# Optimization experiments

Hardware: AMD Instinct MI355X
Metric: run time of the kernel (lower is better)

## Reference

```python
import jax, jax.numpy as jnp
import numpy as np

B, T, IN, H = 4096, 100, 140, 256


def setup_inputs() -> dict:
    key = jax.random.key(0)
    ks = jax.random.split(key, 13)
    s = 1.0 / np.sqrt(H)  # PyTorch LSTM/Linear default init scale
    u = lambda k, shape: jax.random.uniform(k, shape, jnp.float32, -s, s)
    return {
        "x": jax.random.normal(ks[0], (B, T, IN), jnp.float32),
        # LSTM layer 0 (input 140 -> hidden 256), PyTorch gate order i,f,g,o
        "W_ih0": u(ks[1], (4 * H, IN)),
        "W_hh0": u(ks[2], (4 * H, H)),
        "b_ih0": u(ks[3], (4 * H,)),
        "b_hh0": u(ks[4], (4 * H,)),
        # LSTM layer 1 (hidden 256 -> hidden 256)
        "W_ih1": u(ks[5], (4 * H, H)),
        "W_hh1": u(ks[6], (4 * H, H)),
        "b_ih1": u(ks[7], (4 * H,)),
        "b_hh1": u(ks[8], (4 * H,)),
        # advantage MLP: Linear(256,256) -> ReLU -> Linear(256,1)
        "W_a1": u(ks[9], (H, H)),
        "b_a1": u(ks[10], (H,)),
        "W_a2": u(ks[11], (1, H)),
        "b_a2": u(ks[12], (1,)),
    }


def _lstm_cell(xt, h, c, W_ih, W_hh, b):
    # xt: (B, in), h/c: (B, H). PyTorch gate order: i, f, g, o.
    g = xt @ W_ih.T + h @ W_hh.T + b
    i, f, gg, o = jnp.split(g, 4, axis=-1)
    c_new = jax.nn.sigmoid(f) * c + jax.nn.sigmoid(i) * jnp.tanh(gg)
    h_new = jax.nn.sigmoid(o) * jnp.tanh(c_new)
    return h_new, c_new


def reference(x, W_ih0, W_hh0, b_ih0, b_hh0, W_ih1, W_hh1, b_ih1, b_hh1,
              W_a1, b_a1, W_a2, b_a2):
    Bx = x.shape[0]
    b0 = b_ih0 + b_hh0
    b1 = b_ih1 + b_hh1

    def step(carry, xt):
        h0, c0, h1, c1 = carry
        h0, c0 = _lstm_cell(xt, h0, c0, W_ih0, W_hh0, b0)
        h1, c1 = _lstm_cell(h0, h1, c1, W_ih1, W_hh1, b1)
        a = jax.nn.relu(h1 @ W_a1.T + b_a1) @ W_a2.T + b_a2  # (B, 1)
        return (h0, c0, h1, c1), a[:, 0]

    init = tuple(jnp.zeros((Bx, H), x.dtype) for _ in range(4))
    _, outs = jax.lax.scan(step, init, jnp.swapaxes(x, 0, 1))  # (T, B)
    # Faithful to torch.cat(outputs).view(B, -1): flatten in t-major order,
    # then reshape to (B, T) (this scrambles batch/time exactly as the original).
    return outs.reshape(Bx, -1)
```

## Files before the change

kernel.cpp:

```cpp
#include <hip/hip_runtime.h>
#include <cstdint>
#include <cstddef>

#define T_STEPS 100
#define IN_DIM  140
#define HDIM    256
#define BTOT    4096
#define MROWS   16
#define NBLK    (BTOT/MROWS)
#define NTHR    512

typedef _Float16 f16;
typedef _Float16 f16x8 __attribute__((ext_vector_type(8)));
typedef float    f32x4 __attribute__((ext_vector_type(4)));

#define NS0 13
#define NS1 16
#define NSA 8
#define E0 (NS0*64*512)
#define E1 (NS1*64*512)
#define EA (NSA*16*512)
#define F16TOT (E0+E1+EA)
#define EB 2048
#define PREP_TOT (F16TOT+EB)

#define ACOLS 680
#define H0COL 160
#define H1COL 416

__device__ __forceinline__ float sigmoidf_(float x) {
    return 1.0f / (1.0f + __expf(-x));
}
__device__ __forceinline__ float tanhf_(float x) {
    return 1.0f - 2.0f / (__expf(2.0f * x) + 1.0f);
}

__global__ void prep(const float* __restrict__ Wih0, const float* __restrict__ Whh0,
                     const float* __restrict__ bih0, const float* __restrict__ bhh0,
                     const float* __restrict__ Wih1, const float* __restrict__ Whh1,
                     const float* __restrict__ bih1, const float* __restrict__ bhh1,
                     const float* __restrict__ Wa1,  f16* __restrict__ wsf,
                     float* __restrict__ wsb)
{
    int idx = blockIdx.x * 256 + threadIdx.x;
    if (idx < E0) {
        int e = idx & 7, l = (idx >> 3) & 63, fi = idx >> 9;
        int nt = fi & 63, ks = fi >> 6;
        int k = ks * 32 + ((l >> 4) << 3) + e;
        int n = nt * 16 + (l & 15);
        float v = (k < 160) ? (k < IN_DIM ? Wih0[n * IN_DIM + k] : 0.f)
                            : Whh0[n * HDIM + (k - 160)];
        wsf[idx] = (f16)v;
    } else if (idx < E0 + E1) {
        int i2 = idx - E0;
        int e = i2 & 7, l = (i2 >> 3) & 63, fi = i2 >> 9;
        int nt = fi & 63, ks = fi >> 6;
        int k = ks * 32 + ((l >> 4) << 3) + e;
        int n = nt * 16 + (l & 15);
        float v = (k < HDIM) ? Wih1[n * HDIM + k] : Whh1[n * HDIM + (k - HDIM)];
        wsf[idx] = (f16)v;
    } else if (idx < F16TOT) {
        int i3 = idx - (E0 + E1);
        int e = i3 & 7, l = (i3 >> 3) & 63, fi = i3 >> 9;
        int nt = fi & 15, ks = fi >> 4;
        int k = ks * 32 + ((l >> 4) << 3) + e;
        int j = nt * 16 + (l & 15);
        wsf[idx] = (f16)Wa1[j * HDIM + k];
    } else if (idx < PREP_TOT) {
        int i4 = idx - F16TOT;
        if (i4 < 1024) wsb[i4] = bih0[i4] + bhh0[i4];
        else           wsb[i4] = bih1[i4 - 1024] + bhh1[i4 - 1024];
    }
}

#define GLOAD_LDS(gsrc, ldst)                                              \
    __builtin_amdgcn_global_load_lds(                                      \
        (const __attribute__((address_space(1))) void*)(gsrc),             \
        (__attribute__((address_space(3))) void*)(ldst), 16, 0, 0)

#define BAR_LG do { asm volatile("s_waitcnt lgkmcnt(0)" ::: "memory");     \
                    __builtin_amdgcn_sched_barrier(0);                     \
                    __builtin_amdgcn_s_barrier();                          \
                    __builtin_amdgcn_sched_barrier(0); } while (0)

__device__ __forceinline__ f16x8 ldfrag(const f16* base, int f, int w, int l) {
    return *(const f16x8*)(base + ((size_t)(((f >> 1) << 4) + 2 * w + (f & 1)) << 9) + l * 8);
}

__global__ __launch_bounds__(NTHR) void lstm_mfma(
    const float* __restrict__ x, const f16* __restrict__ wsf,
    const float* __restrict__ wsb, const float* __restrict__ Wa2,
    const float* __restrict__ ba1, const float* __restrict__ ba2,
    float* __restrict__ out)
{
    __shared__ __align__(16) f16 A[MROWS][ACOLS];
    __shared__ __align__(16) f16 advL[8 * 16 * 512];
    __shared__ float red[8][MROWS];

    const int tid = threadIdx.x;
    const int l   = tid & 63;
    const int w   = tid >> 6;
    const int lm  = l & 15;
    const int lk  = (l >> 4) << 3;
    const int m0  = (l >> 4) << 2;
    const int row0 = blockIdx.x * MROWS;

    const f16* W0 = wsf;
    const f16* W1 = wsf + E0;
    const f16* WA = wsf + E0 + E1;

    for (int i = tid; i < MROWS * ACOLS; i += NTHR) ((f16*)A)[i] = (f16)0.f;

    const int u0 = (2 * w) * 16 + lm;
    const int u1 = (2 * w + 1) * 16 + lm;
    float b0v[2][4], b1v[2][4];
    #pragma unroll
    for (int g = 0; g < 4; g++) {
        b0v[0][g] = wsb[g * 256 + u0];          b0v[1][g] = wsb[g * 256 + u1];
        b1v[0][g] = wsb[1024 + g * 256 + u0];   b1v[1][g] = wsb[1024 + g * 256 + u1];
    }
    const float bAv[2]  = { ba1[u0], ba1[u1] };
    const float wa2v[2] = { Wa2[u0], Wa2[u1] };
    const float ba2v    = ba2[0];

    #pragma unroll
    for (int fi = 0; fi < 16; fi++) {
        const f16* src = WA + ((size_t)(((fi >> 1) << 4) + 2 * w + (fi & 1)) << 9) + l * 8;
        GLOAD_LDS(src, advL + (size_t)(w * 16 + fi) * 512);
    }

    float c0s[2][4], c1s[2][4];
    #pragma unroll
    for (int q = 0; q < 2; q++)
        #pragma unroll
        for (int r = 0; r < 4; r++) { c0s[q][r] = 0.f; c1s[q][r] = 0.f; }

    for (int i = tid; i < MROWS * IN_DIM; i += NTHR) {
        int b = i / IN_DIM, k = i - b * IN_DIM;
        A[b][k] = (f16)x[(size_t)(row0 + b) * (T_STEPS * IN_DIM) + k];
    }
    f16x8 cur[8];
    #pragma unroll
    for (int f = 0; f < 8; f++) cur[f] = ldfrag(W0, f, w, l);

    __syncthreads();

    #pragma unroll 1
    for (int t = 0; t < T_STEPS; t++) {
        f32x4 acc[2][4];
        #pragma unroll
        for (int q = 0; q < 2; q++)
            #pragma unroll
            for (int g = 0; g < 4; g++) {
                float b = b0v[q][g];
                acc[q][g] = (f32x4){b, b, b, b};
            }
        #pragma unroll 1
        for (int ks = 0; ks < NS0; ks++) {
            const f16* nb = (ks < NS0 - 1) ? (W0 + (size_t)(ks + 1) * (64 * 512)) : W1;
            f16x8 nxt[8];
            #pragma unroll
            for (int f = 0; f < 8; f++) nxt[f] = ldfrag(nb, f, w, l);
            f16x8 a0 = *(const f16x8*)&A[lm][ks * 32 + lk];
            #pragma unroll
            for (int g = 0; g < 4; g++)
                #pragma unroll
                for (int q = 0; q < 2; q++)
                    acc[q][g] = __builtin_amdgcn_mfma_f32_16x16x32_f16(a0, cur[g * 2 + q], acc[q][g], 0, 0, 0);
            #pragma unroll
            for (int f = 0; f < 8; f++) cur[f] = nxt[f];
        }

        f16 hnew[2][4];
        #pragma unroll
        for (int q = 0; q < 2; q++)
            #pragma unroll
            for (int r = 0; r < 4; r++) {
                float ig = sigmoidf_(acc[q][0][r]);
                float fg = sigmoidf_(acc[q][1][r]);
                float gv = tanhf_   (acc[q][2][r]);
                float og = sigmoidf_(acc[q][3][r]);
                float c  = fmaf(fg, c0s[q][r], ig * gv);
                c0s[q][r] = c;
                hnew[q][r] = (f16)(og * tanhf_(c));
            }
        BAR_LG;
        #pragma unroll
        for (int r = 0; r < 4; r++) {
            A[m0 + r][H0COL + u0] = hnew[0][r];
            A[m0 + r][H0COL + u1] = hnew[1][r];
        }
        BAR_LG;

        #pragma unroll
        for (int q = 0; q < 2; q++)
            #pragma unroll
            for (int g = 0; g < 4; g++) {
                float b = b1v[q][g];
                acc[q][g] = (f32x4){b, b, b, b};
            }
        #pragma unroll 1
        for (int ks = 0; ks < NS1; ks++) {
            const f16* nb = (ks < NS1 - 1) ? (W1 + (size_t)(ks + 1) * (64 * 512)) : W0;
            f16x8 nxt[8];
            #pragma unroll
            for (int f = 0; f < 8; f++) nxt[f] = ldfrag(nb, f, w, l);
            f16x8 a0 = *(const f16x8*)&A[lm][H0COL + ks * 32 + lk];
            #pragma unroll
            for (int g = 0; g < 4; g++)
                #pragma unroll
                for (int q = 0; q < 2; q++)
                    acc[q][g] = __builtin_amdgcn_mfma_f32_16x16x32_f16(a0, cur[g * 2 + q], acc[q][g], 0, 0, 0);
            #pragma unroll
            for (int f = 0; f < 8; f++) cur[f] = nxt[f];
        }

        #pragma unroll
        for (int q = 0; q < 2; q++)
            #pragma unroll
            for (int r = 0; r < 4; r++) {
                float ig = sigmoidf_(acc[q][0][r]);
                float fg = sigmoidf_(acc[q][1][r]);
                float gv = tanhf_   (acc[q][2][r]);
                float og = sigmoidf_(acc[q][3][r]);
                float c  = fmaf(fg, c1s[q][r], ig * gv);
                c1s[q][r] = c;
                hnew[q][r] = (f16)(og * tanhf_(c));
            }
        BAR_LG;
        #pragma unroll
        for (int r = 0; r < 4; r++) {
            A[m0 + r][H1COL + u0] = hnew[0][r];
            A[m0 + r][H1COL + u1] = hnew[1][r];
        }
        BAR_LG;

        f32x4 accA[2];
        #pragma unroll
        for (int q = 0; q < 2; q++) {
            float b = bAv[q];
            accA[q] = (f32x4){b, b, b, b};
        }
        #pragma unroll
        for (int ks = 0; ks < NSA; ks++) {
            f16x8 a0 = *(const f16x8*)&A[lm][H1COL + ks * 32 + lk];
            f16x8 bf0 = *(const f16x8*)(advL + (size_t)(w * 16 + 2 * ks + 0) * 512 + l * 8);
            f16x8 bf1 = *(const f16x8*)(advL + (size_t)(w * 16 + 2 * ks + 1) * 512 + l * 8);
            accA[0] = __builtin_amdgcn_mfma_f32_16x16x32_f16(a0, bf0, accA[0], 0, 0, 0);
            accA[1] = __builtin_amdgcn_mfma_f32_16x16x32_f16(a0, bf1, accA[1], 0, 0, 0);
        }

        {
            const int tn = (t + 1 < T_STEPS) ? (t + 1) : t;
            for (int i = tid; i < MROWS * IN_DIM; i += NTHR) {
                int b = i / IN_DIM, k = i - b * IN_DIM;
                A[b][k] = (f16)x[(size_t)(row0 + b) * (T_STEPS * IN_DIM) + (size_t)tn * IN_DIM + k];
            }
        }

        float s[4];
        #pragma unroll
        for (int r = 0; r < 4; r++)
            s[r] = fmaxf(accA[0][r], 0.f) * wa2v[0] + fmaxf(accA[1][r], 0.f) * wa2v[1];
        #pragma unroll
        for (int msk = 1; msk < 16; msk <<= 1)
            #pragma unroll
            for (int r = 0; r < 4; r++)
                s[r] += __shfl_xor(s[r], msk, 64);
        if (lm == 0) {
            #pragma unroll
            for (int r = 0; r < 4; r++) red[w][m0 + r] = s[r];
        }
        BAR_LG;
        if (tid < MROWS) {
            float o = ba2v;
            #pragma unroll
            for (int w2 = 0; w2 < 8; w2++) o += red[w2][tid];
            out[(size_t)t * BTOT + row0 + tid] = o;
        }
    }
}

extern "C" void kernel_launch(void* const* d_in, const int* in_sizes, int n_in,
                              void* d_out, int out_size, void* d_ws, size_t ws_size,
                              hipStream_t stream)
{
    const float* x    = (const float*)d_in[0];
    const float* Wih0 = (const float*)d_in[1];
    const float* Whh0 = (const float*)d_in[2];
    const float* bih0 = (const float*)d_in[3];
    const float* bhh0 = (const float*)d_in[4];
    const float* Wih1 = (const float*)d_in[5];
    const float* Whh1 = (const float*)d_in[6];
    const float* bih1 = (const float*)d_in[7];
    const float* bhh1 = (const float*)d_in[8];
    const float* Wa1  = (const float*)d_in[9];
    const float* ba1  = (const float*)d_in[10];
    const float* Wa2  = (const float*)d_in[11];
    const float* ba2  = (const float*)d_in[12];

    f16*   wsf = (f16*)d_ws;
    float* wsb = (float*)((char*)d_ws + (size_t)F16TOT * sizeof(f16));
    float* out = (float*)d_out;

    hipLaunchKernelGGL(prep, dim3(PREP_TOT / 256), dim3(256), 0, stream,
                       Wih0, Whh0, bih0, bhh0, Wih1, Whh1, bih1, bhh1, Wa1, wsf, wsb);
    hipLaunchKernelGGL(lstm_mfma, dim3(NBLK), dim3(NTHR), 0, stream,
                       x, wsf, wsb, Wa2, ba1, ba2, out);
}
```

Baseline: 1.998 ms.

## Double-buffer LSTM weight fragments two k-slices ahead and set waves_per_eu

Replaces the single-slice register prefetch (cur/nxt copy) with two alternating register buffers. Each global load now has a full k-slice of MFMA work to hide behind, and the register copy is gone. The k-loops are unrolled by two, and the boundary slices are hand-sequenced so the next layer's first two slices are prefetched. A waves_per_eu(2) attribute is added to steer register allocation. The extra fragment registers raise VGPR pressure, and any slip in the prefetch ordering at the layer boundaries would use the wrong weights.

```diff
diff --git a/kernel.cpp b/kernel.cpp
--- a/kernel.cpp
+++ b/kernel.cpp
@@ -23,6 +23,7 @@
 #define F16TOT (E0+E1+EA)
 #define EB 2048
 #define PREP_TOT (F16TOT+EB)
+#define SL (64*512)
 
 #define ACOLS 680
 #define H0COL 160
@@ -87,7 +88,9 @@
     return *(const f16x8*)(base + ((size_t)(((f >> 1) << 4) + 2 * w + (f & 1)) << 9) + l * 8);
 }
 
-__global__ __launch_bounds__(NTHR) void lstm_mfma(
+__global__ __launch_bounds__(NTHR)
+__attribute__((amdgpu_waves_per_eu(2)))
+void lstm_mfma(
     const float* __restrict__ x, const f16* __restrict__ wsf,
     const float* __restrict__ wsb, const float* __restrict__ Wa2,
     const float* __restrict__ ba1, const float* __restrict__ ba2,
@@ -139,9 +142,26 @@
         int b = i / IN_DIM, k = i - b * IN_DIM;
         A[b][k] = (f16)x[(size_t)(row0 + b) * (T_STEPS * IN_DIM) + k];
     }
-    f16x8 cur[8];
-    #pragma unroll
-    for (int f = 0; f < 8; f++) cur[f] = ldfrag(W0, f, w, l);
+
+    f16x8 bsE[8], bsO[8];
+
+#define LDSETX(ARR, BASE)                                                  \
+    do { _Pragma("unroll")                                                 \
+         for (int f = 0; f < 8; f++) ARR[f] = ldfrag((BASE), f, w, l);     \
+    } while (0)
+
+#define MFMA_SX(ARR, COL)                                                  \
+    do { f16x8 a0 = *(const f16x8*)&A[lm][(COL) + lk];                     \
+         _Pragma("unroll")                                                 \
+         for (int g = 0; g < 4; g++)                                       \
+             _Pragma("unroll")                                             \
+             for (int q = 0; q < 2; q++)                                   \
+                 acc[q][g] = __builtin_amdgcn_mfma_f32_16x16x32_f16(       \
+                     a0, ARR[g * 2 + q], acc[q][g], 0, 0, 0);              \
+    } while (0)
+
+    LDSETX(bsE, W0 + 0 * SL);
+    LDSETX(bsO, W0 + 1 * SL);
 
     __syncthreads();
 
@@ -156,20 +176,13 @@
                 acc[q][g] = (f32x4){b, b, b, b};
             }
         #pragma unroll 1
-        for (int ks = 0; ks < NS0; ks++) {
-            const f16* nb = (ks < NS0 - 1) ? (W0 + (size_t)(ks + 1) * (64 * 512)) : W1;
-            f16x8 nxt[8];
-            #pragma unroll
-            for (int f = 0; f < 8; f++) nxt[f] = ldfrag(nb, f, w, l);
-            f16x8 a0 = *(const f16x8*)&A[lm][ks * 32 + lk];
-            #pragma unroll
-            for (int g = 0; g < 4; g++)
-                #pragma unroll
-                for (int q = 0; q < 2; q++)
-                    acc[q][g] = __builtin_amdgcn_mfma_f32_16x16x32_f16(a0, cur[g * 2 + q], acc[q][g], 0, 0, 0);
-            #pragma unroll
-            for (int f = 0; f < 8; f++) cur[f] = nxt[f];
-        }
+        for (int j = 0; j < 5; j++) {
+            MFMA_SX(bsE, (2 * j) * 32);     LDSETX(bsE, W0 + (size_t)(2 * j + 2) * SL);
+            MFMA_SX(bsO, (2 * j + 1) * 32); LDSETX(bsO, W0 + (size_t)(2 * j + 3) * SL);
+        }
+        MFMA_SX(bsE, 10 * 32);  LDSETX(bsE, W0 + 12 * SL);
+        MFMA_SX(bsO, 11 * 32);  LDSETX(bsO, W1 + 1 * SL);
+        MFMA_SX(bsE, 12 * 32);  LDSETX(bsE, W1 + 0 * SL);
 
         f16 hnew[2][4];
         #pragma unroll
@@ -200,20 +213,12 @@
                 acc[q][g] = (f32x4){b, b, b, b};
             }
         #pragma unroll 1
-        for (int ks = 0; ks < NS1; ks++) {
-            const f16* nb = (ks < NS1 - 1) ? (W1 + (size_t)(ks + 1) * (64 * 512)) : W0;
-            f16x8 nxt[8];
-            #pragma unroll
-            for (int f = 0; f < 8; f++) nxt[f] = ldfrag(nb, f, w, l);
-            f16x8 a0 = *(const f16x8*)&A[lm][H0COL + ks * 32 + lk];
-            #pragma unroll
-            for (int g = 0; g < 4; g++)
-                #pragma unroll
-                for (int q = 0; q < 2; q++)
-                    acc[q][g] = __builtin_amdgcn_mfma_f32_16x16x32_f16(a0, cur[g * 2 + q], acc[q][g], 0, 0, 0);
-            #pragma unroll
-            for (int f = 0; f < 8; f++) cur[f] = nxt[f];
-        }
+        for (int j = 0; j < 7; j++) {
+            MFMA_SX(bsE, H0COL + (2 * j) * 32);     LDSETX(bsE, W1 + (size_t)(2 * j + 2) * SL);
+            MFMA_SX(bsO, H0COL + (2 * j + 1) * 32); LDSETX(bsO, W1 + (size_t)(2 * j + 3) * SL);
+        }
+        MFMA_SX(bsE, H0COL + 14 * 32);  LDSETX(bsE, W0 + 0 * SL);
+        MFMA_SX(bsO, H0COL + 15 * 32);  LDSETX(bsO, W0 + 1 * SL);
 
         #pragma unroll
         for (int q = 0; q < 2; q++)
@@ -279,6 +284,8 @@
             out[(size_t)t * BTOT + row0 + tid] = o;
         }
     }
+#undef LDSETX
+#undef MFMA_SX
 }
 
 extern "C" void kernel_launch(void* const* d_in, const int* in_sizes, int n_in,
```

Measured after the change: 1.854 ms (median of 2 runs). 7.2% less time.
